# Performance work log

Hardware: AMD Instinct MI355X
Metric: run time of the kernel (lower is better)

Reference implementation:

```python
import jax, jax.numpy as jnp
import numpy as np

ALPHA = 0.9       # synapse decay
BETA = 0.85       # membrane decay
THRESHOLD = 1.0
SIM_T = 100       # simulation timesteps
SCALE = 100.0     # SuperSpike surrogate scale

@jax.custom_vjp
def spike(x):
    # Heaviside step with SuperSpike surrogate gradient
    return (x > 0).astype(x.dtype)

def _spike_fwd(x):
    return spike(x), x

def _spike_bwd(x, g):
    return (g / (SCALE * jnp.abs(x) + 1.0) ** 2,)

spike.defvjp(_spike_fwd, _spike_bwd)


def setup_inputs() -> dict:
    key = jax.random.key(0)
    k1, k2, k3, k4 = jax.random.split(key, 4)
    input_data = jax.random.uniform(k1, (32768, 128), dtype=jnp.float32)
    # weights ~ N(0, weight_scale/sqrt(fan_in))
    W0 = jax.random.normal(k2, (128, 256), dtype=jnp.float32) * (1.0 / np.sqrt(128).astype(np.float32))
    W1 = jax.random.normal(k3, (256, 256), dtype=jnp.float32) * (1.0 / np.sqrt(256).astype(np.float32))
    W2 = jax.random.normal(k4, (256, 8), dtype=jnp.float32) * (1.0 / np.sqrt(256).astype(np.float32))
    return {"input_data": input_data, "W0": W0, "W1": W1, "W2": W2}


def reference(input_data, W0, W1, W2):
    Ws = (W0, W1, W2)
    B = input_data.shape[0]
    dtype = input_data.dtype
    # constant encoding uses a detached copy of the input each step
    inp = jax.lax.stop_gradient(input_data)

    syn0 = tuple(jnp.zeros((B, W.shape[1]), dtype) for W in Ws)
    mem0 = tuple(jnp.zeros((B, W.shape[1]), dtype) for W in Ws)

    n_layers = len(Ws)

    def step(carry, _):
        syn, mem = carry
        prev = inp
        new_syn, new_mem = [], []
        for l in range(n_layers):
            h = prev @ Ws[l]                         # [B, n_l]
            if l < n_layers - 1:
                mthr = mem[l] - THRESHOLD
                out = spike(mthr)                    # surrogate-grad step
                # reset signal has no gradient path in the original
                rst = jax.lax.stop_gradient((mthr > 0).astype(dtype))
            else:
                out = None                           # output layer never spikes (potential decoding)
                rst = jnp.zeros_like(mem[l])
            new_syn.append(ALPHA * syn[l] + h)
            # membrane update uses the OLD synaptic current (pre-update)
            new_mem.append(BETA * mem[l] + syn[l] - rst)
            prev = out
        return (tuple(new_syn), tuple(new_mem)), None

    (syn, mem), _ = jax.lax.scan(step, (syn0, mem0), None, length=SIM_T)
    # decoding == 'potential': membrane potential of output layer at final step
    return mem[-1]
```

## Files before the change

kernel.cpp:

```cpp
#include <hip/hip_runtime.h>


typedef _Float16 f16;
typedef _Float16 f16x8 __attribute__((ext_vector_type(8)));
typedef float    f32x4 __attribute__((ext_vector_type(4)));
typedef int      i32x4 __attribute__((ext_vector_type(4)));
typedef unsigned int u32;
typedef unsigned long long u64;

#define SIM_T   100
#define MROWS   16
#define BLOCKSZ 512
#define RECIP2048 4.8828125e-4f

#define MFMA16(a, b, c) __builtin_amdgcn_mfma_f32_16x16x32_f16((a), (b), (c), 0, 0, 0)

__global__ __launch_bounds__(BLOCKSZ, 2)
void snn_fused(const float* __restrict__ input,
               const float* __restrict__ W0,
               const float* __restrict__ W1,
               const float* __restrict__ W2,
               float* __restrict__ out)
{
    __shared__ __align__(16) char spk[2][8192];
    __shared__ float h2acc[MROWS * 8];
    __shared__ float ctab[SIM_T];

    const int tid  = threadIdx.x;
    const int wv   = tid >> 6;
    const int ln   = tid & 63;
    const int mrow = ln & 15;
    const int g    = ln >> 4;
    const int row0 = blockIdx.x * MROWS;
    const int n0   = wv * 32;

    if (tid < MROWS * 8) h2acc[tid] = 0.0f;
    if (tid < SIM_T) {
        const float n = (float)(SIM_T - 1 - tid);
        ctab[tid] = 20.0f * (exp2f(n * -0.15200309344504997f)
                           - exp2f(n * -0.23446525363702297f));
    }

    float* instage = (float*)&spk[0][0];
    #pragma unroll
    for (int i = 0; i < 4; ++i)
        instage[i * BLOCKSZ + tid] = input[(size_t)row0 * 128 + i * BLOCKSZ + tid];
    __syncthreads();

    f16x8 xh[4], xl[4];
    #pragma unroll
    for (int kc = 0; kc < 4; ++kc) {
        const float* p = instage + mrow * 128 + kc * 32 + g * 8;
        f16x8 vh, vl;
        #pragma unroll
        for (int e = 0; e < 8; ++e) {
            const float x = p[e];
            const f16 h = (f16)x;
            vh[e] = h;
            vl[e] = (f16)((x - (float)h) * 2048.0f);
        }
        xh[kc] = vh; xl[kc] = vl;
    }

    f32x4 h0a[2], h0b[2];
    #pragma unroll
    for (int nt = 0; nt < 2; ++nt) { h0a[nt] = (f32x4){0,0,0,0}; h0b[nt] = (f32x4){0,0,0,0}; }
    #pragma unroll
    for (int nt = 0; nt < 2; ++nt) {
        const int col = n0 + nt * 16 + mrow;
        #pragma unroll
        for (int kc = 0; kc < 4; ++kc) {
            const int kb = kc * 32 + g * 8;
            f16x8 bh, bl;
            #pragma unroll
            for (int e = 0; e < 8; ++e) {
                const float w = W0[(kb + e) * 256 + col];
                const f16 h = (f16)w;
                bh[e] = h;
                bl[e] = (f16)((w - (float)h) * 2048.0f);
            }
            h0a[nt] = MFMA16(xh[kc], bh, h0a[nt]);
            h0b[nt] = MFMA16(xh[kc], bl, h0b[nt]);
            h0b[nt] = MFMA16(xl[kc], bh, h0b[nt]);
        }
    }

    float H0c[8], syn0[8], mem0[8];
    #pragma unroll
    for (int nt = 0; nt < 2; ++nt)
        #pragma unroll
        for (int q = 0; q < 4; ++q) {
            H0c[nt * 4 + q]  = h0a[nt][q] + RECIP2048 * h0b[nt][q];
            syn0[nt * 4 + q] = 0.0f;
            mem0[nt * 4 + q] = 0.0f;
        }

    f16x8 whi[2][8], wlo[2][8];
    #pragma unroll
    for (int nt = 0; nt < 2; ++nt) {
        const int col = n0 + nt * 16 + mrow;
        #pragma unroll
        for (int kc = 0; kc < 8; ++kc) {
            const int kb = kc * 32 + g * 8;
            f16x8 vh, vl;
            #pragma unroll
            for (int e = 0; e < 8; ++e) {
                const float w = W1[(kb + e) * 256 + col];
                const f16 h = (f16)w;
                vh[e] = h;
                vl[e] = (f16)((w - (float)h) * 2048.0f);
            }
            whi[nt][kc] = vh; wlo[nt][kc] = vl;
        }
    }

    int wba;
    {
        const int slot = wv * 4 + g;
        wba = (slot * 16 + ((mrow + slot) & 15)) * 16;
    }
    const int shamt = ((mrow >> 2) & 1) * 16 + (g & 1) * 8;
    int ra[8];
    #pragma unroll
    for (int kc = 0; kc < 8; ++kc) {
        const int slot = kc * 4 + g;
        ra[kc] = (slot * 16 + ((mrow + slot) & 15)) * 16;
    }

    float syn1[8], mem1[8], Zc[8];
    #pragma unroll
    for (int i = 0; i < 8; ++i) { syn1[i] = 0.0f; mem1[i] = 0.0f; Zc[i] = 0.0f; }

    __syncthreads();

    char* spkbase = &spk[0][0];
    int bufoff = 0;

    #pragma unroll 1
    for (int t = 0; t < SIM_T; ++t) {
        u64 bal[8];
        #pragma unroll
        for (int i = 0; i < 8; ++i) {
            const float m = mem0[i], s = syn0[i];
            const bool fire = m > 1.0f;
            bal[i] = __ballot(fire);
            const float f = fire ? 1.0f : 0.0f;
            mem0[i] = fmaf(0.85f, m, s) - f;
            syn0[i] = fmaf(0.9f, s, H0c[i]);
        }
        {
            const int rq = mrow & 3;
            const u64 s01 = (rq & 1) ? bal[1] : bal[0];
            const u64 s23 = (rq & 1) ? bal[3] : bal[2];
            const u64 sA  = (rq & 2) ? s23 : s01;
            const u64 s45 = (rq & 1) ? bal[5] : bal[4];
            const u64 s67 = (rq & 1) ? bal[7] : bal[6];
            const u64 sB  = (rq & 2) ? s67 : s45;
            const u64 w   = (g & 2) ? sB : sA;
            const u32 hlf = (mrow & 8) ? (u32)(w >> 32) : (u32)w;
            const u32 bits = (hlf >> shamt) & 0xFFu;
            i32x4 pkv;
            #pragma unroll
            for (int p = 0; p < 4; ++p) {
                const u32 tb = bits >> (2 * p);
                pkv[p] = (int)(((tb & 1u) ? 0x3C00u : 0u) |
                               ((tb & 2u) ? 0x3C000000u : 0u));
            }
            *(i32x4*)(spkbase + bufoff + wba) = pkv;
        }
        __syncthreads();

        f32x4 ah[2], al[2];
        ah[0] = (f32x4){0,0,0,0}; ah[1] = (f32x4){0,0,0,0};
        al[0] = (f32x4){0,0,0,0}; al[1] = (f32x4){0,0,0,0};
        #pragma unroll
        for (int kc = 0; kc < 8; ++kc) {
            const f16x8 a = *(const f16x8*)(spkbase + bufoff + ra[kc]);
            ah[0] = MFMA16(a, whi[0][kc], ah[0]);
            al[0] = MFMA16(a, wlo[0][kc], al[0]);
            ah[1] = MFMA16(a, whi[1][kc], ah[1]);
            al[1] = MFMA16(a, wlo[1][kc], al[1]);
        }

        const float ctau = ctab[t];
        #pragma unroll
        for (int nt = 0; nt < 2; ++nt)
            #pragma unroll
            for (int q = 0; q < 4; ++q) {
                const int i = nt * 4 + q;
                const float h1 = ah[nt][q] + RECIP2048 * al[nt][q];
                const float m = mem1[i], s = syn1[i];
                const bool fire = m > 1.0f;
                const float f = fire ? 1.0f : 0.0f;
                Zc[i]   = fmaf(ctau, f, Zc[i]);
                mem1[i] = fmaf(0.85f, m, s) - f;
                syn1[i] = fmaf(0.9f, s, h1);
            }
        bufoff ^= 8192;
    }

    #pragma unroll
    for (int q = 0; q < 4; ++q) {
        const int r = g * 4 + q;
        const float z0 = Zc[q], z1 = Zc[4 + q];
        const float* w2a = W2 + (n0 + mrow) * 8;
        const float* w2b = W2 + (n0 + 16 + mrow) * 8;
        #pragma unroll
        for (int o = 0; o < 8; ++o)
            atomicAdd(&h2acc[r * 8 + o], z0 * w2a[o] + z1 * w2b[o]);
    }
    __syncthreads();
    if (tid < MROWS * 8)
        out[(size_t)row0 * 8 + tid] = h2acc[tid];
}

extern "C" void kernel_launch(void* const* d_in, const int* in_sizes, int n_in,
                              void* d_out, int out_size, void* d_ws, size_t ws_size,
                              hipStream_t stream) {
    const float* input = (const float*)d_in[0];
    const float* W0    = (const float*)d_in[1];
    const float* W1    = (const float*)d_in[2];
    const float* W2    = (const float*)d_in[3];
    float* outp = (float*)d_out;
    const int B    = in_sizes[0] / 128;
    const int grid = B / MROWS;
    snn_fused<<<grid, BLOCKSZ, 0, stream>>>(input, W0, W1, W2, outp);
}
```

Baseline: 1.161 ms.

## Split columns across 16 waves per block, recurrently compute decay coefficient

Doubles the block to 1024 threads so each wave owns 16 output columns of the 256-wide hidden layers instead of 32. This halves per-thread MFMA work, weight registers and state per timestep, and raises the occupancy target. The spike ballot packing and LDS layout are reworked to write 8-byte chunks. The precomputed decay-coefficient table is replaced by two geometric recurrences, which may drift slightly in float, and the W2 atomics are staggered to spread bank conflicts. More waves per block means more participants in each per-step __syncthreads barrier.

```diff
diff --git a/kernel.cpp b/kernel.cpp
--- a/kernel.cpp
+++ b/kernel.cpp
@@ -4,18 +4,18 @@
 typedef _Float16 f16;
 typedef _Float16 f16x8 __attribute__((ext_vector_type(8)));
 typedef float    f32x4 __attribute__((ext_vector_type(4)));
-typedef int      i32x4 __attribute__((ext_vector_type(4)));
 typedef unsigned int u32;
+typedef u32      u32x2 __attribute__((ext_vector_type(2)));
 typedef unsigned long long u64;
 
 #define SIM_T   100
 #define MROWS   16
-#define BLOCKSZ 512
+#define BLOCKSZ 1024
 #define RECIP2048 4.8828125e-4f
 
 #define MFMA16(a, b, c) __builtin_amdgcn_mfma_f32_16x16x32_f16((a), (b), (c), 0, 0, 0)
 
-__global__ __launch_bounds__(BLOCKSZ, 2)
+__global__ __launch_bounds__(BLOCKSZ, 4)
 void snn_fused(const float* __restrict__ input,
                const float* __restrict__ W0,
                const float* __restrict__ W1,
@@ -24,7 +24,6 @@
 {
     __shared__ __align__(16) char spk[2][8192];
     __shared__ float h2acc[MROWS * 8];
-    __shared__ float ctab[SIM_T];
 
     const int tid  = threadIdx.x;
     const int wv   = tid >> 6;
@@ -32,19 +31,13 @@
     const int mrow = ln & 15;
     const int g    = ln >> 4;
     const int row0 = blockIdx.x * MROWS;
-    const int n0   = wv * 32;
+    const int n0   = wv * 16;
 
     if (tid < MROWS * 8) h2acc[tid] = 0.0f;
-    if (tid < SIM_T) {
-        const float n = (float)(SIM_T - 1 - tid);
-        ctab[tid] = 20.0f * (exp2f(n * -0.15200309344504997f)
-                           - exp2f(n * -0.23446525363702297f));
-    }
 
     float* instage = (float*)&spk[0][0];
-    #pragma unroll
-    for (int i = 0; i < 4; ++i)
-        instage[i * BLOCKSZ + tid] = input[(size_t)row0 * 128 + i * BLOCKSZ + tid];
+    instage[tid]        = input[(size_t)row0 * 128 + tid];
+    instage[tid + 1024] = input[(size_t)row0 * 128 + tid + 1024];
     __syncthreads();
 
     f16x8 xh[4], xl[4];
@@ -62,12 +55,9 @@
         xh[kc] = vh; xl[kc] = vl;
     }
 
-    f32x4 h0a[2], h0b[2];
-    #pragma unroll
-    for (int nt = 0; nt < 2; ++nt) { h0a[nt] = (f32x4){0,0,0,0}; h0b[nt] = (f32x4){0,0,0,0}; }
-    #pragma unroll
-    for (int nt = 0; nt < 2; ++nt) {
-        const int col = n0 + nt * 16 + mrow;
+    f32x4 h0a = (f32x4){0, 0, 0, 0}, h0b = (f32x4){0, 0, 0, 0};
+    {
+        const int col = n0 + mrow;
         #pragma unroll
         for (int kc = 0; kc < 4; ++kc) {
             const int kb = kc * 32 + g * 8;
@@ -79,26 +69,23 @@
                 bh[e] = h;
                 bl[e] = (f16)((w - (float)h) * 2048.0f);
             }
-            h0a[nt] = MFMA16(xh[kc], bh, h0a[nt]);
-            h0b[nt] = MFMA16(xh[kc], bl, h0b[nt]);
-            h0b[nt] = MFMA16(xl[kc], bh, h0b[nt]);
-        }
-    }
-
-    float H0c[8], syn0[8], mem0[8];
-    #pragma unroll
-    for (int nt = 0; nt < 2; ++nt)
-        #pragma unroll
-        for (int q = 0; q < 4; ++q) {
-            H0c[nt * 4 + q]  = h0a[nt][q] + RECIP2048 * h0b[nt][q];
-            syn0[nt * 4 + q] = 0.0f;
-            mem0[nt * 4 + q] = 0.0f;
-        }
-
-    f16x8 whi[2][8], wlo[2][8];
-    #pragma unroll
-    for (int nt = 0; nt < 2; ++nt) {
-        const int col = n0 + nt * 16 + mrow;
+            h0a = MFMA16(xh[kc], bh, h0a);
+            h0b = MFMA16(xh[kc], bl, h0b);
+            h0b = MFMA16(xl[kc], bh, h0b);
+        }
+    }
+
+    float H0c[4], syn0[4], mem0[4];
+    #pragma unroll
+    for (int q = 0; q < 4; ++q) {
+        H0c[q]  = h0a[q] + RECIP2048 * h0b[q];
+        syn0[q] = 0.0f;
+        mem0[q] = 0.0f;
+    }
+
+    f16x8 whi[8], wlo[8];
+    {
+        const int col = n0 + mrow;
         #pragma unroll
         for (int kc = 0; kc < 8; ++kc) {
             const int kb = kc * 32 + g * 8;
@@ -110,104 +97,96 @@
                 vh[e] = h;
                 vl[e] = (f16)((w - (float)h) * 2048.0f);
             }
-            whi[nt][kc] = vh; wlo[nt][kc] = vl;
+            whi[kc] = vh; wlo[kc] = vl;
         }
     }
 
     int wba;
     {
-        const int slot = wv * 4 + g;
-        wba = (slot * 16 + ((mrow + slot) & 15)) * 16;
-    }
-    const int shamt = ((mrow >> 2) & 1) * 16 + (g & 1) * 8;
-    int ra[8];
-    #pragma unroll
-    for (int kc = 0; kc < 8; ++kc) {
+        const int slot = wv * 2 + (g >> 1);
+        wba = (slot * 16 + ((mrow + slot) & 15)) * 16 + (g & 1) * 8;
+    }
+    const int shamt2 = (mrow >> 2) * 16 + g * 4;
+    int ra[4];
+    #pragma unroll
+    for (int kc = 0; kc < 4; ++kc) {
         const int slot = kc * 4 + g;
         ra[kc] = (slot * 16 + ((mrow + slot) & 15)) * 16;
     }
 
-    float syn1[8], mem1[8], Zc[8];
-    #pragma unroll
-    for (int i = 0; i < 8; ++i) { syn1[i] = 0.0f; mem1[i] = 0.0f; Zc[i] = 0.0f; }
+    float syn1[4], mem1[4], Zc[4];
+    #pragma unroll
+    for (int q = 0; q < 4; ++q) { syn1[q] = 0.0f; mem1[q] = 0.0f; Zc[q] = 0.0f; }
+
+    float U = 20.0f * exp2f(-15.0483062f);
+    float V = 20.0f * exp2f(-23.2120601f);
 
     __syncthreads();
 
-    char* spkbase = &spk[0][0];
-    int bufoff = 0;
-
+    int buf = 0;
     #pragma unroll 1
     for (int t = 0; t < SIM_T; ++t) {
-        u64 bal[8];
-        #pragma unroll
-        for (int i = 0; i < 8; ++i) {
-            const float m = mem0[i], s = syn0[i];
+        u64 bal[4];
+        #pragma unroll
+        for (int q = 0; q < 4; ++q) {
+            const float m = mem0[q], s = syn0[q];
             const bool fire = m > 1.0f;
-            bal[i] = __ballot(fire);
+            bal[q] = __ballot(fire);
             const float f = fire ? 1.0f : 0.0f;
-            mem0[i] = fmaf(0.85f, m, s) - f;
-            syn0[i] = fmaf(0.9f, s, H0c[i]);
+            mem0[q] = fmaf(0.85f, m, s) - f;
+            syn0[q] = fmaf(0.9f, s, H0c[q]);
         }
         {
             const int rq = mrow & 3;
-            const u64 s01 = (rq & 1) ? bal[1] : bal[0];
-            const u64 s23 = (rq & 1) ? bal[3] : bal[2];
-            const u64 sA  = (rq & 2) ? s23 : s01;
-            const u64 s45 = (rq & 1) ? bal[5] : bal[4];
-            const u64 s67 = (rq & 1) ? bal[7] : bal[6];
-            const u64 sB  = (rq & 2) ? s67 : s45;
-            const u64 w   = (g & 2) ? sB : sA;
-            const u32 hlf = (mrow & 8) ? (u32)(w >> 32) : (u32)w;
-            const u32 bits = (hlf >> shamt) & 0xFFu;
-            i32x4 pkv;
+            const u64 b01 = (rq & 1) ? bal[1] : bal[0];
+            const u64 b23 = (rq & 1) ? bal[3] : bal[2];
+            const u64 bw  = (rq & 2) ? b23 : b01;
+            const u32 bits = (u32)(bw >> shamt2) & 0xFu;
+            u32x2 pk;
+            pk.x = ((bits & 1u) ? 0x3C00u : 0u) | ((bits & 2u) ? 0x3C000000u : 0u);
+            pk.y = ((bits & 4u) ? 0x3C00u : 0u) | ((bits & 8u) ? 0x3C000000u : 0u);
+            *(u32x2*)(&spk[0][0] + buf + wba) = pk;
+        }
+        __syncthreads();
+
+        f32x4 ah = (f32x4){0, 0, 0, 0}, al = (f32x4){0, 0, 0, 0};
+        const char* base = &spk[0][0] + buf;
+        #pragma unroll
+        for (int kc = 0; kc < 8; ++kc) {
+            const f16x8 a = *(const f16x8*)(base + ra[kc & 3] + (kc >> 2) * 4096);
+            ah = MFMA16(a, whi[kc], ah);
+            al = MFMA16(a, wlo[kc], al);
+        }
+
+        const float ctau = U - V;
+        U *= 1.1111112f;
+        V *= 1.1764706f;
+
+        #pragma unroll
+        for (int q = 0; q < 4; ++q) {
+            const float h1 = ah[q] + RECIP2048 * al[q];
+            const float m = mem1[q], s = syn1[q];
+            const bool fire = m > 1.0f;
+            const float f = fire ? 1.0f : 0.0f;
+            Zc[q]   = fmaf(ctau, f, Zc[q]);
+            mem1[q] = fmaf(0.85f, m, s) - f;
+            syn1[q] = fmaf(0.9f, s, h1);
+        }
+        buf ^= 8192;
+    }
+
+    {
+        const float* w2 = W2 + (n0 + mrow) * 8;
+        #pragma unroll
+        for (int q = 0; q < 4; ++q) {
+            const int r = g * 4 + q;
+            const float z = Zc[q];
             #pragma unroll
-            for (int p = 0; p < 4; ++p) {
-                const u32 tb = bits >> (2 * p);
-                pkv[p] = (int)(((tb & 1u) ? 0x3C00u : 0u) |
-                               ((tb & 2u) ? 0x3C000000u : 0u));
+            for (int oo = 0; oo < 8; ++oo) {
+                const int o = (oo + mrow) & 7;
+                atomicAdd(&h2acc[r * 8 + o], z * w2[o]);
             }
-            *(i32x4*)(spkbase + bufoff + wba) = pkv;
-        }
-        __syncthreads();
-
-        f32x4 ah[2], al[2];
-        ah[0] = (f32x4){0,0,0,0}; ah[1] = (f32x4){0,0,0,0};
-        al[0] = (f32x4){0,0,0,0}; al[1] = (f32x4){0,0,0,0};
-        #pragma unroll
-        for (int kc = 0; kc < 8; ++kc) {
-            const f16x8 a = *(const f16x8*)(spkbase + bufoff + ra[kc]);
-            ah[0] = MFMA16(a, whi[0][kc], ah[0]);
-            al[0] = MFMA16(a, wlo[0][kc], al[0]);
-            ah[1] = MFMA16(a, whi[1][kc], ah[1]);
-            al[1] = MFMA16(a, wlo[1][kc], al[1]);
-        }
-
-        const float ctau = ctab[t];
-        #pragma unroll
-        for (int nt = 0; nt < 2; ++nt)
-            #pragma unroll
-            for (int q = 0; q < 4; ++q) {
-                const int i = nt * 4 + q;
-                const float h1 = ah[nt][q] + RECIP2048 * al[nt][q];
-                const float m = mem1[i], s = syn1[i];
-                const bool fire = m > 1.0f;
-                const float f = fire ? 1.0f : 0.0f;
-                Zc[i]   = fmaf(ctau, f, Zc[i]);
-                mem1[i] = fmaf(0.85f, m, s) - f;
-                syn1[i] = fmaf(0.9f, s, h1);
-            }
-        bufoff ^= 8192;
-    }
-
-    #pragma unroll
-    for (int q = 0; q < 4; ++q) {
-        const int r = g * 4 + q;
-        const float z0 = Zc[q], z1 = Zc[4 + q];
-        const float* w2a = W2 + (n0 + mrow) * 8;
-        const float* w2b = W2 + (n0 + 16 + mrow) * 8;
-        #pragma unroll
-        for (int o = 0; o < 8; ++o)
-            atomicAdd(&h2acc[r * 8 + o], z0 * w2a[o] + z1 * w2b[o]);
+        }
     }
     __syncthreads();
     if (tid < MROWS * 8)
```

Result: slower. 1.239 ms (+6.7%).
